# Performance work log

Measured on AMD Instinct MI355X. Metric: run time of the kernel, lower is better.

The kernel has to match this reference:

```python
import jax, jax.numpy as jnp
import numpy as np

TOP_K = 2


def setup_inputs() -> dict:
    key = jax.random.key(0)
    ks = jax.random.split(key, 10)
    D, F, E = 1024, 4096, 8
    s = 0.02  # realistic init scale, keeps activations stable
    return {
        "x": jax.random.normal(ks[0], (2, 4096, D), dtype=jnp.float32),
        "gate_w": jax.random.normal(ks[1], (E, D), dtype=jnp.float32) * s,
        "w1": jax.random.normal(ks[2], (E, F, D), dtype=jnp.float32) * s,
        "b1": jax.random.normal(ks[3], (E, F), dtype=jnp.float32) * s,
        "w2": jax.random.normal(ks[4], (E, D, F), dtype=jnp.float32) * s,
        "b2": jax.random.normal(ks[5], (E, D), dtype=jnp.float32) * s,
        "sw1": jax.random.normal(ks[6], (F, D), dtype=jnp.float32) * s,
        "sb1": jax.random.normal(ks[7], (F,), dtype=jnp.float32) * s,
        "sw2": jax.random.normal(ks[8], (D, F), dtype=jnp.float32) * s,
        "sb2": jax.random.normal(ks[9], (D,), dtype=jnp.float32) * s,
    }


def _ffn(x, w1, b1, w2, b2):
    # GELU(x @ W1^T + b1) @ W2^T + b2 ; torch F.gelu default = exact (erf)
    h = jax.nn.gelu(x @ w1.T + b1, approximate=False)
    return h @ w2.T + b2


def reference(x, gate_w, w1, b1, w2, b2, sw1, sb1, sw2, sb2):
    B, S, D = x.shape
    E = gate_w.shape[0]
    xt = x.reshape(-1, D)  # [T, D]

    # MoEGate: linear -> softmax -> top-k (weights not renormalized)
    scores = jax.nn.softmax(xt @ gate_w.T, axis=-1)  # [T, E]
    topk_w, topk_idx = jax.lax.top_k(scores, TOP_K)  # [T, K]

    # moe_infer: per-expert FFN, combine with top-k gate weights.
    # Reference form: dense per-expert compute, masked combine (combine sum is
    # permutation-invariant so top-k ordering does not matter).
    out = jnp.zeros_like(xt)
    for e in range(E):
        we = jnp.sum(jnp.where(topk_idx == e, topk_w, 0.0), axis=-1)  # [T]
        out = out + we[:, None] * _ffn(xt, w1[e], b1[e], w2[e], b2[e])

    # shared expert applied to the identity input
    out = out + _ffn(xt, sw1, sb1, sw2, sb2)
    return out.reshape(B, S, D)
```

## Files before the change

kernel.cpp:

```cpp
#include <hip/hip_runtime.h>
#include <hip/hip_bf16.h>

typedef __bf16 bf16_t;
typedef __bf16 bf16x8 __attribute__((ext_vector_type(8)));
typedef float  f32x4  __attribute__((ext_vector_type(4)));

static constexpr int TT = 8192;
static constexpr int DD = 1024;
static constexpr int FF = 4096;
static constexpr int NSLOT = 2 * TT;

#define R_COUNTS 0
#define R_OFFSET 8
#define R_TSTART 17
#define R_TOTAL  34
#define R_INTS   40

#define GLL(g, l) __builtin_amdgcn_global_load_lds( \
    (__attribute__((address_space(1))) void*)(g), \
    (__attribute__((address_space(3))) void*)(l), 16, 0, 0)

__device__ __forceinline__ float fast_gelu(float v) {
  float t = -1.5957691216f * v - 0.0713548162f * (v * v * v);
  return v / (1.f + __expf(t));
}

__global__ __launch_bounds__(256) void cvt_f32_bf16(const float* __restrict__ src,
                                                    bf16_t* __restrict__ dst, int n8) {
  int i = blockIdx.x * 256 + threadIdx.x;
  if (i >= n8) return;
  const float4* s = reinterpret_cast<const float4*>(src) + (size_t)i * 2;
  float4 a = s[0], b = s[1];
  bf16x8 v;
  v[0] = (bf16_t)a.x; v[1] = (bf16_t)a.y; v[2] = (bf16_t)a.z; v[3] = (bf16_t)a.w;
  v[4] = (bf16_t)b.x; v[5] = (bf16_t)b.y; v[6] = (bf16_t)b.z; v[7] = (bf16_t)b.w;
  *reinterpret_cast<bf16x8*>(dst + (size_t)i * 8) = v;
}

__global__ __launch_bounds__(256) void gate_kernel(const float* __restrict__ x,
                                                   const float* __restrict__ gw,
                                                   float* __restrict__ topkw,
                                                   int* __restrict__ slote,
                                                   bf16_t* __restrict__ xb) {
  int wid = threadIdx.x >> 6, lane = threadIdx.x & 63;
  int t = blockIdx.x * 4 + wid;
  const float4* xv = reinterpret_cast<const float4*>(x + (size_t)t * DD) + lane * 4;
  const float4* gv = reinterpret_cast<const float4*>(gw);
  float acc[8];
  float4 xs[4];
#pragma unroll
  for (int e = 0; e < 8; ++e) acc[e] = 0.f;
#pragma unroll
  for (int i = 0; i < 4; ++i) {
    float4 xi = xv[i];
    xs[i] = xi;
#pragma unroll
    for (int e = 0; e < 8; ++e) {
      float4 g = gv[e * 256 + lane * 4 + i];
      acc[e] += xi.x * g.x + xi.y * g.y + xi.z * g.z + xi.w * g.w;
    }
  }
  {
    bf16x8 lo, hi;
    lo[0]=(bf16_t)xs[0].x; lo[1]=(bf16_t)xs[0].y; lo[2]=(bf16_t)xs[0].z; lo[3]=(bf16_t)xs[0].w;
    lo[4]=(bf16_t)xs[1].x; lo[5]=(bf16_t)xs[1].y; lo[6]=(bf16_t)xs[1].z; lo[7]=(bf16_t)xs[1].w;
    hi[0]=(bf16_t)xs[2].x; hi[1]=(bf16_t)xs[2].y; hi[2]=(bf16_t)xs[2].z; hi[3]=(bf16_t)xs[2].w;
    hi[4]=(bf16_t)xs[3].x; hi[5]=(bf16_t)xs[3].y; hi[6]=(bf16_t)xs[3].z; hi[7]=(bf16_t)xs[3].w;
    bf16_t* d = xb + (size_t)t * DD + lane * 16;
    *reinterpret_cast<bf16x8*>(d) = lo;
    *reinterpret_cast<bf16x8*>(d + 8) = hi;
  }
#pragma unroll
  for (int e = 0; e < 8; ++e)
    for (int off = 32; off; off >>= 1) acc[e] += __shfl_xor(acc[e], off, 64);
  if (lane == 0) {
    float m = acc[0];
#pragma unroll
    for (int e = 1; e < 8; ++e) m = fmaxf(m, acc[e]);
    float p[8], s = 0.f;
#pragma unroll
    for (int e = 0; e < 8; ++e) { p[e] = expf(acc[e] - m); s += p[e]; }
    float inv = 1.f / s;
#pragma unroll
    for (int e = 0; e < 8; ++e) p[e] *= inv;
    int e1 = 0; float b1v = p[0];
#pragma unroll
    for (int e = 1; e < 8; ++e) if (p[e] > b1v) { b1v = p[e]; e1 = e; }
    int e2 = -1; float b2v = -1.f;
#pragma unroll
    for (int e = 0; e < 8; ++e) if (e != e1 && p[e] > b2v) { b2v = p[e]; e2 = e; }
    topkw[2 * t] = b1v;  topkw[2 * t + 1] = b2v;
    slote[2 * t] = e1;   slote[2 * t + 1] = e2;
  }
}

__global__ __launch_bounds__(256) void hist_kernel(const int* __restrict__ slote,
                                                   int* __restrict__ routing) {
  __shared__ int red[256];
  const int e = blockIdx.x;
  const int t = threadIdx.x;
  int cnt = 0;
  for (int base = 0; base < NSLOT; base += 256)
    cnt += (slote[base + t] == e) ? 1 : 0;
  red[t] = cnt;
  __syncthreads();
  for (int s = 128; s; s >>= 1) {
    if (t < s) red[t] += red[t + s];
    __syncthreads();
  }
  if (t == 0) routing[R_COUNTS + e] = red[0];
}

__global__ void scan_kernel(int* __restrict__ routing) {
  int off = 0, tt = 0;
  for (int e = 0; e < 8; ++e) {
    routing[R_OFFSET + e] = off;
    routing[R_TSTART + e] = tt;
    int c = routing[R_COUNTS + e];
    off += c;
    tt += (c + 127) >> 7;
  }
  routing[R_OFFSET + 8] = off;
  routing[R_TSTART + 8] = tt;
  routing[R_TOTAL] = tt;
}

__global__ __launch_bounds__(256) void scatter_kernel(const int* __restrict__ slote,
                                                      const int* __restrict__ routing,
                                                      int* __restrict__ perm,
                                                      int* __restrict__ pos) {
  __shared__ int wtot[4];
  const int e = blockIdx.x;
  const int t = threadIdx.x;
  const int lane = t & 63, wid = t >> 6;
  int running = routing[R_OFFSET + e];
  for (int base = 0; base < NSLOT; base += 256) {
    int s = base + t;
    bool m = (slote[s] == e);
    unsigned long long mask = __ballot(m);
    int wrank = __popcll(mask & ((1ull << lane) - 1ull));
    if (lane == 0) wtot[wid] = __popcll(mask);
    __syncthreads();
    int wpre = 0;
#pragma unroll
    for (int w = 0; w < 4; ++w) if (w < wid) wpre += wtot[w];
    int tot = wtot[0] + wtot[1] + wtot[2] + wtot[3];
    if (m) {
      int pp = running + wpre + wrank;
      perm[pp] = s;
      pos[s] = pp;
    }
    running += tot;
    __syncthreads();
  }
}

__global__ __launch_bounds__(256) void combine_kernel(const bf16_t* __restrict__ slotb,
                                                      const int* __restrict__ pos,
                                                      float* __restrict__ out) {
  int idx = blockIdx.x * 256 + threadIdx.x;
  int t = idx >> 7;
  int c = (idx & 127) << 3;
  int p0 = pos[2 * t], p1 = pos[2 * t + 1];
  bf16x8 s0 = *reinterpret_cast<const bf16x8*>(&slotb[(size_t)p0 * DD + c]);
  bf16x8 s1 = *reinterpret_cast<const bf16x8*>(&slotb[(size_t)p1 * DD + c]);
  float* o = &out[(size_t)t * DD + c];
  float4 o0 = *reinterpret_cast<const float4*>(o);
  float4 o1 = *reinterpret_cast<const float4*>(o + 4);
  o0.x += (float)s0[0] + (float)s1[0];
  o0.y += (float)s0[1] + (float)s1[1];
  o0.z += (float)s0[2] + (float)s1[2];
  o0.w += (float)s0[3] + (float)s1[3];
  o1.x += (float)s0[4] + (float)s1[4];
  o1.y += (float)s0[5] + (float)s1[5];
  o1.z += (float)s0[6] + (float)s1[6];
  o1.w += (float)s0[7] + (float)s1[7];
  *reinterpret_cast<float4*>(o) = o0;
  *reinterpret_cast<float4*>(o + 4) = o1;
}

template <int MODE>
__global__ __launch_bounds__(256, 4) void gemm_kernel(
    const bf16_t* __restrict__ A, const bf16_t* __restrict__ Bw,
    const float* __restrict__ bias, bf16_t* __restrict__ Hout,
    float* __restrict__ out, const int* __restrict__ routing,
    const int* __restrict__ perm, const float* __restrict__ topkw) {
  constexpr bool EXPERT = (MODE < 2);
  constexpr int K = (MODE == 0 || MODE == 2) ? 1024 : 4096;
  constexpr int NTOT = (MODE == 0 || MODE == 2) ? 4096 : 1024;
  constexpr int NT = NTOT / 128;
  constexpr int NKT = K / 64;
  constexpr int OUTD = (MODE == 0 || MODE == 2) ? FF : DD;

  __shared__ __align__(16) bf16_t lds[16384];
  __shared__ float wrow[128];

  const int t = threadIdx.x;
  const int lane = t & 63;
  const int wid = t >> 6;
  const int wm = wid >> 1;
  const int wn = wid & 1;

  const int nwg = gridDim.x;
  const int q = nwg >> 3, r = nwg & 7;
  const int xcd = blockIdx.x & 7, bi = blockIdx.x >> 3;
  const int swz = (xcd < r ? xcd * (q + 1) : r * (q + 1) + (xcd - r) * q) + bi;
  const int mt = swz / NT;
  const int nt = swz & (NT - 1);

  int row0, valid, eidx = 0;
  if constexpr (EXPERT) {
    if (mt >= routing[R_TOTAL]) return;
    int e = 0;
    while (e < 7 && routing[R_TSTART + e + 1] <= mt) ++e;
    eidx = e;
    int lm = mt - routing[R_TSTART + e];
    row0 = routing[R_OFFSET + e] + lm * 128;
    valid = min(128, routing[R_COUNTS + e] - lm * 128);
  } else {
    row0 = mt * 128;
    valid = 128;
  }

  const bf16_t* Bexp = Bw + (EXPERT ? (size_t)eidx * NTOT * K : 0);
  const float* biasp = bias + (EXPERT ? eidx * NTOT : 0);

  const int sub = t >> 3;
  const int lc = (t & 7) ^ (sub & 7);
  const bf16_t* aS[4];
  const bf16_t* bS[4];
#pragma unroll
  for (int i = 0; i < 4; ++i) {
    int lr = sub + i * 32;
    int gr;
    if constexpr (MODE == 0) {
      gr = perm[row0 + min(lr, valid - 1)] >> 1;
    } else if constexpr (MODE == 1) {
      gr = row0 + min(lr, valid - 1);
    } else {
      gr = row0 + lr;
    }
    aS[i] = A + (size_t)gr * K + lc * 8;
    bS[i] = Bexp + (size_t)(nt * 128 + lr) * K + lc * 8;
  }
  bf16_t* const aD = lds + (sub << 6) + ((t & 7) << 3);
  bf16_t* const bD = aD + 8192;

  const int l15 = lane & 15, lq = lane >> 4;

  f32x4 acc[4][4];
#pragma unroll
  for (int m = 0; m < 4; ++m)
#pragma unroll
    for (int n = 0; n < 4; ++n) acc[m][n] = f32x4{0.f, 0.f, 0.f, 0.f};

  for (int kt = 0; kt < NKT; ++kt) {
    const size_t kof = (size_t)kt * 64;
#pragma unroll
    for (int i = 0; i < 4; ++i) {
      GLL(aS[i] + kof, aD + i * 2048);
      GLL(bS[i] + kof, bD + i * 2048);
    }
    __syncthreads();

#pragma unroll
    for (int kk = 0; kk < 2; ++kk) {
      bf16x8 af[4], bfr[4];
#pragma unroll
      for (int m = 0; m < 4; ++m) {
        int ra = wm * 64 + m * 16 + l15;
        int ph = (kk * 4 + lq) ^ (ra & 7);
        af[m] = *reinterpret_cast<const bf16x8*>(&lds[ra * 64 + ph * 8]);
      }
#pragma unroll
      for (int n = 0; n < 4; ++n) {
        int rb = wn * 64 + n * 16 + l15;
        int ph = (kk * 4 + lq) ^ (rb & 7);
        bfr[n] = *reinterpret_cast<const bf16x8*>(&lds[8192 + rb * 64 + ph * 8]);
      }
      __builtin_amdgcn_s_setprio(1);
#pragma unroll
      for (int m = 0; m < 4; ++m)
#pragma unroll
        for (int n = 0; n < 4; ++n)
          acc[m][n] = __builtin_amdgcn_mfma_f32_16x16x32_bf16(af[m], bfr[n], acc[m][n], 0, 0, 0);
      __builtin_amdgcn_s_setprio(0);
    }
    __syncthreads();
  }

  if constexpr (MODE == 1) {
    if (t < 128) wrow[t] = topkw[perm[row0 + min(t, valid - 1)]];
  }

  float bc[4];
#pragma unroll
  for (int n = 0; n < 4; ++n) bc[n] = biasp[nt * 128 + wn * 64 + n * 16 + l15];

  if constexpr (MODE != 3) {
    bf16_t* scr = lds;
#pragma unroll
    for (int h = 0; h < 2; ++h) {
      __syncthreads();
      if (wm == h) {
#pragma unroll
        for (int m = 0; m < 4; ++m)
#pragma unroll
          for (int n = 0; n < 4; ++n)
#pragma unroll
            for (int rr = 0; rr < 4; ++rr) {
              float v = acc[m][n][rr] + bc[n];
              float o;
              if constexpr (MODE == 1) o = wrow[h * 64 + m * 16 + lq * 4 + rr] * v;
              else                     o = fast_gelu(v);
              scr[(m * 16 + lq * 4 + rr) * 128 + wn * 64 + n * 16 + l15] = (bf16_t)o;
            }
      }
      __syncthreads();
#pragma unroll
      for (int i = 0; i < 4; ++i) {
        int c = t + i * 256;
        int rowp = c >> 4, cc = c & 15;
        int lr = h * 64 + rowp;
        if (lr < valid) {
          bf16x8 v8 = *reinterpret_cast<const bf16x8*>(&scr[rowp * 128 + cc * 8]);
          *reinterpret_cast<bf16x8*>(&Hout[(size_t)(row0 + lr) * OUTD + nt * 128 + cc * 8]) = v8;
        }
      }
    }
  } else {
    float* scr = reinterpret_cast<float*>(lds);
#pragma unroll
    for (int h = 0; h < 2; ++h) {
      __syncthreads();
      if (wm == h) {
#pragma unroll
        for (int m = 0; m < 4; ++m)
#pragma unroll
          for (int n = 0; n < 4; ++n)
#pragma unroll
            for (int rr = 0; rr < 4; ++rr)
              scr[(m * 16 + lq * 4 + rr) * 128 + wn * 64 + n * 16 + l15] = acc[m][n][rr] + bc[n];
      }
      __syncthreads();
#pragma unroll
      for (int i = 0; i < 8; ++i) {
        int c = t + i * 256;
        int rowp = c >> 5, cc = c & 31;
        int lr = h * 64 + rowp;
        float4 v4 = *reinterpret_cast<const float4*>(&scr[rowp * 128 + cc * 4]);
        *reinterpret_cast<float4*>(&out[(size_t)(row0 + lr) * OUTD + nt * 128 + cc * 4]) = v4;
      }
    }
  }
}

extern "C" void kernel_launch(void* const* d_in, const int* in_sizes, int n_in,
                              void* d_out, int out_size, void* d_ws, size_t ws_size,
                              hipStream_t stream) {
  const float* x   = (const float*)d_in[0];
  const float* gw  = (const float*)d_in[1];
  const float* w1  = (const float*)d_in[2];
  const float* b1  = (const float*)d_in[3];
  const float* w2  = (const float*)d_in[4];
  const float* b2  = (const float*)d_in[5];
  const float* sw1 = (const float*)d_in[6];
  const float* sb1 = (const float*)d_in[7];
  const float* sw2 = (const float*)d_in[8];
  const float* sb2 = (const float*)d_in[9];
  float* out = (float*)d_out;

  char* ws = (char*)d_ws;
  bf16_t* xb    = (bf16_t*)(ws);
  bf16_t* w1b   = (bf16_t*)(ws + ((size_t)16 << 20));
  bf16_t* w2b   = (bf16_t*)(ws + ((size_t)80 << 20));
  bf16_t* sw1b  = (bf16_t*)(ws + ((size_t)144 << 20));
  bf16_t* sw2b  = (bf16_t*)(ws + ((size_t)152 << 20));
  bf16_t* Hbuf  = (bf16_t*)(ws + ((size_t)160 << 20));
  bf16_t* slotb = (bf16_t*)(ws);
  float*  topkw = (float*)(ws + ((size_t)288 << 20));
  int*    slote = (int*)(ws + ((size_t)288 << 20) + 65536);
  int*    perm  = (int*)(ws + ((size_t)288 << 20) + 2 * 65536);
  int*    pos   = (int*)(ws + ((size_t)288 << 20) + 3 * 65536);
  int*    routing = (int*)(ws + ((size_t)288 << 20) + 4 * 65536);

  cvt_f32_bf16<<<(8 * FF * DD / 8 + 255) / 256, 256, 0, stream>>>(w1, w1b, 8 * FF * DD / 8);
  cvt_f32_bf16<<<(8 * DD * FF / 8 + 255) / 256, 256, 0, stream>>>(w2, w2b, 8 * DD * FF / 8);
  cvt_f32_bf16<<<(FF * DD / 8 + 255) / 256, 256, 0, stream>>>(sw1, sw1b, FF * DD / 8);
  cvt_f32_bf16<<<(DD * FF / 8 + 255) / 256, 256, 0, stream>>>(sw2, sw2b, DD * FF / 8);

  gate_kernel<<<TT / 4, 256, 0, stream>>>(x, gw, topkw, slote, xb);
  hist_kernel<<<8, 256, 0, stream>>>(slote, routing);
  scan_kernel<<<1, 1, 0, stream>>>(routing);
  scatter_kernel<<<8, 256, 0, stream>>>(slote, routing, perm, pos);

  gemm_kernel<2><<<64 * 32, 256, 0, stream>>>(xb, sw1b, sb1, Hbuf, out, routing, perm, nullptr);
  gemm_kernel<3><<<64 * 8, 256, 0, stream>>>(Hbuf, sw2b, sb2, nullptr, out, routing, perm, nullptr);
  gemm_kernel<0><<<136 * 32, 256, 0, stream>>>(xb, w1b, b1, Hbuf, out, routing, perm, nullptr);
  gemm_kernel<1><<<136 * 8, 256, 0, stream>>>(Hbuf, w2b, b2, slotb, nullptr, routing, perm, topkw);

  combine_kernel<<<TT * DD / 8 / 256, 256, 0, stream>>>(slotb, pos, out);
}
```

Baseline: 697.9 us.

## Fuse routing kernels and fold expert combine into shared-expert GEMM epilogue

Three routing kernels (histogram, scan, scatter) become one route_kernel. Each of its 8 blocks copies the slot-expert array into LDS, computes all expert counts and offsets itself, and scatters its own expert. The expert GEMMs now run before the shared-expert GEMMs, and the shared down-projection epilogue adds the two per-token expert slot rows straight into the output, so the separate combine kernel and its extra read and rewrite of the output are gone. The trade-offs are redundant counting in every route block, a large LDS footprint there, and the slot buffer moved to overlap the already-consumed w1 bf16 region.

```diff
diff --git a/kernel.cpp b/kernel.cpp
--- a/kernel.cpp
+++ b/kernel.cpp
@@ -2,6 +2,7 @@
 #include <hip/hip_bf16.h>
 
 typedef __bf16 bf16_t;
+typedef __bf16 bf16x4 __attribute__((ext_vector_type(4)));
 typedef __bf16 bf16x8 __attribute__((ext_vector_type(8)));
 typedef float  f32x4  __attribute__((ext_vector_type(4)));
 
@@ -94,49 +95,63 @@
   }
 }
 
-__global__ __launch_bounds__(256) void hist_kernel(const int* __restrict__ slote,
-                                                   int* __restrict__ routing) {
+__global__ __launch_bounds__(256) void route_kernel(const int* __restrict__ slote,
+                                                    int* __restrict__ routing,
+                                                    int* __restrict__ perm,
+                                                    int* __restrict__ pos) {
+  __shared__ int sl[NSLOT > 16384 ? 1 : 16384];
   __shared__ int red[256];
-  const int e = blockIdx.x;
-  const int t = threadIdx.x;
-  int cnt = 0;
-  for (int base = 0; base < NSLOT; base += 256)
-    cnt += (slote[base + t] == e) ? 1 : 0;
-  red[t] = cnt;
-  __syncthreads();
-  for (int s = 128; s; s >>= 1) {
-    if (t < s) red[t] += red[t + s];
-    __syncthreads();
-  }
-  if (t == 0) routing[R_COUNTS + e] = red[0];
-}
-
-__global__ void scan_kernel(int* __restrict__ routing) {
-  int off = 0, tt = 0;
-  for (int e = 0; e < 8; ++e) {
-    routing[R_OFFSET + e] = off;
-    routing[R_TSTART + e] = tt;
-    int c = routing[R_COUNTS + e];
-    off += c;
-    tt += (c + 127) >> 7;
-  }
-  routing[R_OFFSET + 8] = off;
-  routing[R_TSTART + 8] = tt;
-  routing[R_TOTAL] = tt;
-}
-
-__global__ __launch_bounds__(256) void scatter_kernel(const int* __restrict__ slote,
-                                                      const int* __restrict__ routing,
-                                                      int* __restrict__ perm,
-                                                      int* __restrict__ pos) {
   __shared__ int wtot[4];
   const int e = blockIdx.x;
   const int t = threadIdx.x;
   const int lane = t & 63, wid = t >> 6;
-  int running = routing[R_OFFSET + e];
+
+  for (int i = t; i < NSLOT; i += 256) sl[i] = slote[i];
+  __syncthreads();
+
+  int cnt[8];
+#pragma unroll
+  for (int ee = 0; ee < 8; ++ee) cnt[ee] = 0;
+  for (int i = t; i < NSLOT; i += 256) ++cnt[sl[i]];
+
+  int tot[8];
+#pragma unroll
+  for (int ee = 0; ee < 8; ++ee) {
+    red[t] = cnt[ee];
+    __syncthreads();
+    for (int s = 128; s; s >>= 1) {
+      if (t < s) red[t] += red[t + s];
+      __syncthreads();
+    }
+    tot[ee] = red[0];
+    __syncthreads();
+  }
+
+  int offarr[9], tstart[9];
+  {
+    int off = 0, tts = 0;
+#pragma unroll
+    for (int ee = 0; ee < 8; ++ee) {
+      offarr[ee] = off; tstart[ee] = tts;
+      off += tot[ee]; tts += (tot[ee] + 127) >> 7;
+    }
+    offarr[8] = off; tstart[8] = tts;
+  }
+  if (e == 0 && t == 0) {
+#pragma unroll
+    for (int ee = 0; ee < 8; ++ee) routing[R_COUNTS + ee] = tot[ee];
+#pragma unroll
+    for (int ee = 0; ee < 9; ++ee) {
+      routing[R_OFFSET + ee] = offarr[ee];
+      routing[R_TSTART + ee] = tstart[ee];
+    }
+    routing[R_TOTAL] = tstart[8];
+  }
+
+  int running = offarr[e];
   for (int base = 0; base < NSLOT; base += 256) {
     int s = base + t;
-    bool m = (slote[s] == e);
+    bool m = (sl[s] == e);
     unsigned long long mask = __ballot(m);
     int wrank = __popcll(mask & ((1ull << lane) - 1ull));
     if (lane == 0) wtot[wid] = __popcll(mask);
@@ -144,39 +159,15 @@
     int wpre = 0;
 #pragma unroll
     for (int w = 0; w < 4; ++w) if (w < wid) wpre += wtot[w];
-    int tot = wtot[0] + wtot[1] + wtot[2] + wtot[3];
+    int totb = wtot[0] + wtot[1] + wtot[2] + wtot[3];
     if (m) {
       int pp = running + wpre + wrank;
       perm[pp] = s;
       pos[s] = pp;
     }
-    running += tot;
-    __syncthreads();
-  }
-}
-
-__global__ __launch_bounds__(256) void combine_kernel(const bf16_t* __restrict__ slotb,
-                                                      const int* __restrict__ pos,
-                                                      float* __restrict__ out) {
-  int idx = blockIdx.x * 256 + threadIdx.x;
-  int t = idx >> 7;
-  int c = (idx & 127) << 3;
-  int p0 = pos[2 * t], p1 = pos[2 * t + 1];
-  bf16x8 s0 = *reinterpret_cast<const bf16x8*>(&slotb[(size_t)p0 * DD + c]);
-  bf16x8 s1 = *reinterpret_cast<const bf16x8*>(&slotb[(size_t)p1 * DD + c]);
-  float* o = &out[(size_t)t * DD + c];
-  float4 o0 = *reinterpret_cast<const float4*>(o);
-  float4 o1 = *reinterpret_cast<const float4*>(o + 4);
-  o0.x += (float)s0[0] + (float)s1[0];
-  o0.y += (float)s0[1] + (float)s1[1];
-  o0.z += (float)s0[2] + (float)s1[2];
-  o0.w += (float)s0[3] + (float)s1[3];
-  o1.x += (float)s0[4] + (float)s1[4];
-  o1.y += (float)s0[5] + (float)s1[5];
-  o1.z += (float)s0[6] + (float)s1[6];
-  o1.w += (float)s0[7] + (float)s1[7];
-  *reinterpret_cast<float4*>(o) = o0;
-  *reinterpret_cast<float4*>(o + 4) = o1;
+    running += totb;
+    __syncthreads();
+  }
 }
 
 template <int MODE>
@@ -184,7 +175,8 @@
     const bf16_t* __restrict__ A, const bf16_t* __restrict__ Bw,
     const float* __restrict__ bias, bf16_t* __restrict__ Hout,
     float* __restrict__ out, const int* __restrict__ routing,
-    const int* __restrict__ perm, const float* __restrict__ topkw) {
+    const int* __restrict__ perm, const float* __restrict__ topkw,
+    const int* __restrict__ pos, const bf16_t* __restrict__ slotb) {
   constexpr bool EXPERT = (MODE < 2);
   constexpr int K = (MODE == 0 || MODE == 2) ? 1024 : 4096;
   constexpr int NTOT = (MODE == 0 || MODE == 2) ? 4096 : 1024;
@@ -194,6 +186,7 @@
 
   __shared__ __align__(16) bf16_t lds[16384];
   __shared__ float wrow[128];
+  __shared__ int spos[256];
 
   const int t = threadIdx.x;
   const int lane = t & 63;
@@ -292,6 +285,9 @@
   if constexpr (MODE == 1) {
     if (t < 128) wrow[t] = topkw[perm[row0 + min(t, valid - 1)]];
   }
+  if constexpr (MODE == 3) {
+    spos[t] = pos[2 * row0 + t];
+  }
 
   float bc[4];
 #pragma unroll
@@ -348,7 +344,14 @@
         int c = t + i * 256;
         int rowp = c >> 5, cc = c & 31;
         int lr = h * 64 + rowp;
+        int p0 = spos[2 * lr], p1 = spos[2 * lr + 1];
         float4 v4 = *reinterpret_cast<const float4*>(&scr[rowp * 128 + cc * 4]);
+        bf16x4 s0 = *reinterpret_cast<const bf16x4*>(&slotb[(size_t)p0 * DD + nt * 128 + cc * 4]);
+        bf16x4 s1 = *reinterpret_cast<const bf16x4*>(&slotb[(size_t)p1 * DD + nt * 128 + cc * 4]);
+        v4.x += (float)s0[0] + (float)s1[0];
+        v4.y += (float)s0[1] + (float)s1[1];
+        v4.z += (float)s0[2] + (float)s1[2];
+        v4.w += (float)s0[3] + (float)s1[3];
         *reinterpret_cast<float4*>(&out[(size_t)(row0 + lr) * OUTD + nt * 128 + cc * 4]) = v4;
       }
     }
@@ -377,7 +380,7 @@
   bf16_t* sw1b  = (bf16_t*)(ws + ((size_t)144 << 20));
   bf16_t* sw2b  = (bf16_t*)(ws + ((size_t)152 << 20));
   bf16_t* Hbuf  = (bf16_t*)(ws + ((size_t)160 << 20));
-  bf16_t* slotb = (bf16_t*)(ws);
+  bf16_t* slotb = (bf16_t*)(ws + ((size_t)16 << 20));
   float*  topkw = (float*)(ws + ((size_t)288 << 20));
   int*    slote = (int*)(ws + ((size_t)288 << 20) + 65536);
   int*    perm  = (int*)(ws + ((size_t)288 << 20) + 2 * 65536);
@@ -390,14 +393,10 @@
   cvt_f32_bf16<<<(DD * FF / 8 + 255) / 256, 256, 0, stream>>>(sw2, sw2b, DD * FF / 8);
 
   gate_kernel<<<TT / 4, 256, 0, stream>>>(x, gw, topkw, slote, xb);
-  hist_kernel<<<8, 256, 0, stream>>>(slote, routing);
-  scan_kernel<<<1, 1, 0, stream>>>(routing);
-  scatter_kernel<<<8, 256, 0, stream>>>(slote, routing, perm, pos);
-
-  gemm_kernel<2><<<64 * 32, 256, 0, stream>>>(xb, sw1b, sb1, Hbuf, out, routing, perm, nullptr);
-  gemm_kernel<3><<<64 * 8, 256, 0, stream>>>(Hbuf, sw2b, sb2, nullptr, out, routing, perm, nullptr);
-  gemm_kernel<0><<<136 * 32, 256, 0, stream>>>(xb, w1b, b1, Hbuf, out, routing, perm, nullptr);
-  gemm_kernel<1><<<136 * 8, 256, 0, stream>>>(Hbuf, w2b, b2, slotb, nullptr, routing, perm, topkw);
-
-  combine_kernel<<<TT * DD / 8 / 256, 256, 0, stream>>>(slotb, pos, out);
-}
+  route_kernel<<<8, 256, 0, stream>>>(slote, routing, perm, pos);
+
+  gemm_kernel<0><<<136 * 32, 256, 0, stream>>>(xb, w1b, b1, Hbuf, nullptr, routing, perm, nullptr, nullptr, nullptr);
+  gemm_kernel<1><<<136 * 8, 256, 0, stream>>>(Hbuf, w2b, b2, slotb, nullptr, routing, perm, topkw, nullptr, nullptr);
+  gemm_kernel<2><<<64 * 32, 256, 0, stream>>>(xb, sw1b, sb1, Hbuf, nullptr, routing, perm, nullptr, nullptr, nullptr);
+  gemm_kernel<3><<<64 * 8, 256, 0, stream>>>(Hbuf, sw2b, sb2, nullptr, out, routing, perm, nullptr, pos, slotb);
+}
```

Result: no change. 695.6 us (-0.3%).
